# Kernel tuning notes

Measured on AMD Instinct MI355X. Metric: run time of the kernel, lower is better.

The kernel has to match this reference:

```python
import jax, jax.numpy as jnp
import numpy as np

HEAD_DIM = 128
SCALE = 1.0 / np.sqrt(HEAD_DIM)  # standard 1/sqrt(d) attention scaling


def setup_inputs() -> dict:
    key = jax.random.key(0)
    kq, kk, kv = jax.random.split(key, 3)
    q = jax.random.normal(kq, (2, 32, 2048, HEAD_DIM), dtype=jnp.float16)
    k = jax.random.normal(kk, (2, 8, 2048, HEAD_DIM), dtype=jnp.float16)
    v = jax.random.normal(kv, (2, 8, 2048, HEAD_DIM), dtype=jnp.float16)
    return {"q": q, "k": k, "v": v}


def reference(q, k, v):
    # GQA attention: each of the g = H // KVH query heads in a group attends
    # against the group's single shared K/V head (no K/V duplication).
    b, h, sq, d = q.shape
    kvh = k.shape[1]
    g = h // kvh
    # [b, kvh, g, sq, d] -- group-packed Q, mirroring the kernel's _pack_q
    qg = q.reshape(b, kvh, g, sq, d)
    # fp32 accumulation as in flash-attention kernels
    scores = jnp.einsum(
        'bhgqd,bhkd->bhgqk',
        qg.astype(jnp.float32), k.astype(jnp.float32)) * SCALE
    p = jax.nn.softmax(scores, axis=-1)  # non-causal, full attention
    o = jnp.einsum('bhgqk,bhkd->bhgqd', p, v.astype(jnp.float32))
    return o.reshape(b, h, sq, d).astype(q.dtype)
```

## Files before the change

kernel.cpp:

```cpp
#include <hip/hip_runtime.h>

#define SEQ    2048
#define HD     128
#define BN     64
#define NITER  (SEQ / BN)
#define NKVH   16
#define TILE_E 8192

typedef __fp16 f16x8  __attribute__((ext_vector_type(8)));
typedef float  f32x4  __attribute__((ext_vector_type(4)));
typedef float  f32x16 __attribute__((ext_vector_type(16)));

__device__ __forceinline__ unsigned pkh(float a, float b) {
  auto h = __builtin_amdgcn_cvt_pkrtz(a, b);
  return __builtin_bit_cast(unsigned, h);
}

__device__ __forceinline__ void gl_lds16(const unsigned short* g, unsigned short* l) {
  __builtin_amdgcn_global_load_lds(
      (const __attribute__((address_space(1))) void*)g,
      (__attribute__((address_space(3))) void*)l, 16, 0, 0);
}

__global__ __launch_bounds__(256)
void cvt_kv(const float* __restrict__ K, const float* __restrict__ V,
            unsigned short* __restrict__ Kw, unsigned short* __restrict__ Vw)
{
  __shared__ unsigned short kt[TILE_E];
  __shared__ unsigned short vt[TILE_E];
  const int tid = threadIdx.x;
  const int T   = blockIdx.x;
  const long base = (long)T * TILE_E;

  const int krow = tid >> 2, kq4 = tid & 3;
  const float* kp = K + base + (long)krow * HD + kq4 * 32;
#pragma unroll
  for (int jj = 0; jj < 4; ++jj) {
    float4 e = ((const float4*)kp)[2 * jj];
    float4 o = ((const float4*)kp)[2 * jj + 1];
    int4 ksj;
    ksj.x = (int)pkh(e.x, e.y);
    ksj.y = (int)pkh(e.z, e.w);
    ksj.z = (int)pkh(o.x, o.y);
    ksj.w = (int)pkh(o.z, o.w);
    int j = kq4 * 4 + jj;
    int pos = j ^ (krow & 15);
    *(int4*)(kt + krow * HD + pos * 8) = ksj;
  }
  const int kq = tid >> 4, dc8 = tid & 15;
  const float* vp = V + base + (long)(4 * kq) * HD + dc8 * 8;
  float4 vr[4][2];
#pragma unroll
  for (int r = 0; r < 4; ++r) {
    vr[r][0] = ((const float4*)(vp + r * HD))[0];
    vr[r][1] = ((const float4*)(vp + r * HD))[1];
  }
#pragma unroll
  for (int jd = 0; jd < 8; ++jd) {
    const int hsel = jd >> 2, e = jd & 3;
    uint2 v2;
    v2.x = pkh(((const float*)&vr[0][hsel])[e], ((const float*)&vr[1][hsel])[e]);
    v2.y = pkh(((const float*)&vr[2][hsel])[e], ((const float*)&vr[3][hsel])[e]);
    int d = dc8 * 8 + jd;
    int sw3 = ((d >> 3) ^ d) & 7;
    int pos = (kq >> 1) ^ sw3;
    *(uint2*)(vt + d * 64 + pos * 8 + (kq & 1) * 4) = v2;
  }
  __syncthreads();
  int4* kd = (int4*)(Kw + (long)T * TILE_E);
  int4* vd = (int4*)(Vw + (long)T * TILE_E);
  const int4* ksrc = (const int4*)kt;
  const int4* vsrc = (const int4*)vt;
#pragma unroll
  for (int i = 0; i < 4; ++i) {
    kd[i * 256 + tid] = ksrc[i * 256 + tid];
    vd[i * 256 + tid] = vsrc[i * 256 + tid];
  }
}

__global__ __launch_bounds__(256, 2)
void fa_gqa_kernel(const float* __restrict__ Q,
                   const unsigned short* __restrict__ Kw,
                   const unsigned short* __restrict__ Vw,
                   float* __restrict__ O)
{
  __shared__ unsigned short kt_lds[2][TILE_E];
  __shared__ unsigned short vt_lds[2][TILE_E];

  const int tid  = threadIdx.x;
  const int lane = tid & 63;
  const int w    = tid >> 6;
  const int ml   = lane & 31;
  const int hi   = lane >> 5;
  const bool hib = (hi != 0);

  const int F     = blockIdx.x;
  const int xcd   = F & 7;
  const int s     = F >> 3;
  const int bh    = xcd * 8 + (s >> 4);
  const int qtile = s & 15;

  const int b = bh >> 5;
  const int h = bh & 31;
  const long qrow0 = (long)bh * SEQ + qtile * 128 + w * 32;
  const float* Qw = Q + qrow0 * HD;
  float*       Ow = O + qrow0 * HD;
  const int kvh = b * 8 + (h >> 2);

  f16x8 qf[8];
#pragma unroll
  for (int dc = 0; dc < 8; ++dc) {
    const float4* qp = (const float4*)(Qw + ml * HD + dc * 16 + hi * 8);
    float4 a = qp[0], bq = qp[1];
    int4 t;
    t.x = (int)pkh(a.x, a.y);
    t.y = (int)pkh(a.z, a.w);
    t.z = (int)pkh(bq.x, bq.y);
    t.w = (int)pkh(bq.z, bq.w);
    qf[dc] = __builtin_bit_cast(f16x8, t);
  }

  f32x16 oacc[4];
#pragma unroll
  for (int dt = 0; dt < 4; ++dt)
    oacc[dt] = (f32x16)(0.f);

  float mst = -1e30f;
  float lst = 0.f;

  const float K1 = 0.08838834764831845f * 1.4426950408889634f;

  const unsigned short* kwb = Kw + (long)kvh * NITER * TILE_E;
  const unsigned short* vwb = Vw + (long)kvh * NITER * TILE_E;
  const int woff = w * 2048;

  {
    const unsigned short* ks = kwb + woff + lane * 8;
    const unsigned short* vs = vwb + woff + lane * 8;
#pragma unroll
    for (int c = 0; c < 4; ++c) {
      gl_lds16(ks + c * 512, &kt_lds[0][woff + c * 512]);
      gl_lds16(vs + c * 512, &vt_lds[0][woff + c * 512]);
    }
  }

  for (int it = 0; it < NITER; ++it) {
    const int cur = it & 1;
    __syncthreads();

    if (it + 1 < NITER) {
      const unsigned short* ks = kwb + (long)(it + 1) * TILE_E + woff + lane * 8;
      const unsigned short* vs = vwb + (long)(it + 1) * TILE_E + woff + lane * 8;
      const int nxt = cur ^ 1;
#pragma unroll
      for (int c = 0; c < 4; ++c) {
        gl_lds16(ks + c * 512, &kt_lds[nxt][woff + c * 512]);
        gl_lds16(vs + c * 512, &vt_lds[nxt][woff + c * 512]);
      }
    }

    f32x16 sacc[2];
    sacc[0] = (f32x16)(0.f);
    sacc[1] = (f32x16)(0.f);

#pragma unroll
    for (int dc = 0; dc < 8; ++dc) {
#pragma unroll
      for (int kt = 0; kt < 2; ++kt) {
        int row = kt * 32 + ml;
        int pos = (2 * dc + hi) ^ (row & 15);
        f16x8 af = *(const f16x8*)(kt_lds[cur] + row * HD + pos * 8);
        sacc[kt] = __builtin_amdgcn_mfma_f32_32x32x16_f16(
            af, qf[dc], sacc[kt], 0, 0, 0);
      }
    }

    float x0 = fmaxf(sacc[0][0], sacc[1][0]);
    float x1 = fmaxf(sacc[0][1], sacc[1][1]);
    float x2 = fmaxf(sacc[0][2], sacc[1][2]);
    float x3 = fmaxf(sacc[0][3], sacc[1][3]);
#pragma unroll
    for (int r = 4; r < 16; r += 4) {
      x0 = fmaxf(x0, fmaxf(sacc[0][r + 0], sacc[1][r + 0]));
      x1 = fmaxf(x1, fmaxf(sacc[0][r + 1], sacc[1][r + 1]));
      x2 = fmaxf(x2, fmaxf(sacc[0][r + 2], sacc[1][r + 2]));
      x3 = fmaxf(x3, fmaxf(sacc[0][r + 3], sacc[1][r + 3]));
    }
    float mx = fmaxf(fmaxf(x0, x1), fmaxf(x2, x3));
    mx = fmaxf(mx, __shfl_xor(mx, 32, 64));

    if (__any(mx > mst)) {
      float mnew = fmaxf(mst, mx);
      float alpha = __builtin_amdgcn_exp2f(K1 * (mst - mnew));
      mst = mnew;
      lst *= alpha;
#pragma unroll
      for (int dt = 0; dt < 4; ++dt)
        oacc[dt] *= alpha;
    }

    const float nm = -K1 * mst;
    float p0 = 0.f, p1 = 0.f, p2 = 0.f, p3 = 0.f;
#pragma unroll
    for (int kt = 0; kt < 2; ++kt) {
#pragma unroll
      for (int r = 0; r < 16; r += 4) {
        float e0 = __builtin_amdgcn_exp2f(fmaf(sacc[kt][r + 0], K1, nm));
        float e1 = __builtin_amdgcn_exp2f(fmaf(sacc[kt][r + 1], K1, nm));
        float e2 = __builtin_amdgcn_exp2f(fmaf(sacc[kt][r + 2], K1, nm));
        float e3 = __builtin_amdgcn_exp2f(fmaf(sacc[kt][r + 3], K1, nm));
        sacc[kt][r + 0] = e0; p0 += e0;
        sacc[kt][r + 1] = e1; p1 += e1;
        sacc[kt][r + 2] = e2; p2 += e2;
        sacc[kt][r + 3] = e3; p3 += e3;
      }
    }
    lst += (p0 + p1) + (p2 + p3);

#pragma unroll
    for (int st = 0; st < 4; ++st) {
      const int kt = st >> 1;
      const int R  = 8 * (st & 1);
      unsigned pA0 = pkh(sacc[kt][R + 0], sacc[kt][R + 1]);
      unsigned pA1 = pkh(sacc[kt][R + 2], sacc[kt][R + 3]);
      unsigned pB0 = pkh(sacc[kt][R + 4], sacc[kt][R + 5]);
      unsigned pB1 = pkh(sacc[kt][R + 6], sacc[kt][R + 7]);
      unsigned s0 = hib ? pA0 : pB0;
      unsigned s1 = hib ? pA1 : pB1;
      unsigned r0 = (unsigned)__shfl_xor((int)s0, 32, 64);
      unsigned r1 = (unsigned)__shfl_xor((int)s1, 32, 64);
      int4 bf;
      bf.x = (int)(hib ? r0 : pA0);
      bf.y = (int)(hib ? r1 : pA1);
      bf.z = (int)(hib ? pB0 : r0);
      bf.w = (int)(hib ? pB1 : r1);
      f16x8 pfrag = __builtin_bit_cast(f16x8, bf);
#pragma unroll
      for (int dt = 0; dt < 4; ++dt) {
        int d = dt * 32 + ml;
        int pos = (2 * st + hi) ^ (((d >> 3) ^ d) & 7);
        f16x8 vf = *(const f16x8*)(vt_lds[cur] + d * 64 + pos * 8);
        oacc[dt] = __builtin_amdgcn_mfma_f32_32x32x16_f16(
            vf, pfrag, oacc[dt], 0, 0, 0);
      }
    }
  }

  float lf = lst + __shfl_xor(lst, 32, 64);
  float linv = 1.0f / lf;
#pragma unroll
  for (int dt = 0; dt < 4; ++dt) {
#pragma unroll
    for (int t = 0; t < 4; ++t) {
      f32x4 ov;
      ov[0] = oacc[dt][4 * t + 0] * linv;
      ov[1] = oacc[dt][4 * t + 1] * linv;
      ov[2] = oacc[dt][4 * t + 2] * linv;
      ov[3] = oacc[dt][4 * t + 3] * linv;
      *(f32x4*)(Ow + ml * HD + dt * 32 + 8 * t + 4 * hi) = ov;
    }
  }
}

extern "C" void kernel_launch(void* const* d_in, const int* in_sizes, int n_in,
                              void* d_out, int out_size, void* d_ws, size_t ws_size,
                              hipStream_t stream) {
  const float* q = (const float*)d_in[0];
  const float* k = (const float*)d_in[1];
  const float* v = (const float*)d_in[2];
  float* o = (float*)d_out;
  unsigned short* Kw = (unsigned short*)d_ws;
  unsigned short* Vw = Kw + (long)NKVH * NITER * TILE_E;
  cvt_kv<<<dim3(NKVH * NITER), dim3(256), 0, stream>>>(k, v, Kw, Vw);
  fa_gqa_kernel<<<dim3(1024), dim3(256), 0, stream>>>(q, Kw, Vw, o);
}
```

Baseline: 312.5 us.

## Load V fragments directly from global into registers, use 32x32x8 MFMA for PV

The converter now writes V in a fragment-ready layout straight to global memory, with no LDS staging. The attention kernel drops the V LDS double buffer and loads V fragments from global into registers, prefetching one group ahead. The PV product switches from 32x32x16 to 32x32x8 MFMA so the P fragment comes straight from the accumulator registers without cross-lane shuffles. This saves LDS traffic, the shuffles and LDS capacity, but exposes the kernel to global/L2 load latency inside the loop and doubles the number of PV MFMA instructions.

```diff
diff --git a/kernel.cpp b/kernel.cpp
--- a/kernel.cpp
+++ b/kernel.cpp
@@ -7,6 +7,7 @@
 #define NKVH   16
 #define TILE_E 8192
 
+typedef __fp16 f16x4  __attribute__((ext_vector_type(4)));
 typedef __fp16 f16x8  __attribute__((ext_vector_type(8)));
 typedef float  f32x4  __attribute__((ext_vector_type(4)));
 typedef float  f32x16 __attribute__((ext_vector_type(16)));
@@ -27,7 +28,6 @@
             unsigned short* __restrict__ Kw, unsigned short* __restrict__ Vw)
 {
   __shared__ unsigned short kt[TILE_E];
-  __shared__ unsigned short vt[TILE_E];
   const int tid = threadIdx.x;
   const int T   = blockIdx.x;
   const long base = (long)T * TILE_E;
@@ -47,6 +47,7 @@
     int pos = j ^ (krow & 15);
     *(int4*)(kt + krow * HD + pos * 8) = ksj;
   }
+
   const int kq = tid >> 4, dc8 = tid & 15;
   const float* vp = V + base + (long)(4 * kq) * HD + dc8 * 8;
   float4 vr[4][2];
@@ -55,27 +56,22 @@
     vr[r][0] = ((const float4*)(vp + r * HD))[0];
     vr[r][1] = ((const float4*)(vp + r * HD))[1];
   }
+  uint2* vdst = (uint2*)Vw + (long)T * 2048 + kq * 128 + dc8 * 8;
 #pragma unroll
   for (int jd = 0; jd < 8; ++jd) {
     const int hsel = jd >> 2, e = jd & 3;
     uint2 v2;
     v2.x = pkh(((const float*)&vr[0][hsel])[e], ((const float*)&vr[1][hsel])[e]);
     v2.y = pkh(((const float*)&vr[2][hsel])[e], ((const float*)&vr[3][hsel])[e]);
-    int d = dc8 * 8 + jd;
-    int sw3 = ((d >> 3) ^ d) & 7;
-    int pos = (kq >> 1) ^ sw3;
-    *(uint2*)(vt + d * 64 + pos * 8 + (kq & 1) * 4) = v2;
-  }
+    vdst[jd] = v2;
+  }
+
   __syncthreads();
   int4* kd = (int4*)(Kw + (long)T * TILE_E);
-  int4* vd = (int4*)(Vw + (long)T * TILE_E);
   const int4* ksrc = (const int4*)kt;
-  const int4* vsrc = (const int4*)vt;
-#pragma unroll
-  for (int i = 0; i < 4; ++i) {
+#pragma unroll
+  for (int i = 0; i < 4; ++i)
     kd[i * 256 + tid] = ksrc[i * 256 + tid];
-    vd[i * 256 + tid] = vsrc[i * 256 + tid];
-  }
 }
 
 __global__ __launch_bounds__(256, 2)
@@ -85,14 +81,12 @@
                    float* __restrict__ O)
 {
   __shared__ unsigned short kt_lds[2][TILE_E];
-  __shared__ unsigned short vt_lds[2][TILE_E];
 
   const int tid  = threadIdx.x;
   const int lane = tid & 63;
   const int w    = tid >> 6;
   const int ml   = lane & 31;
   const int hi   = lane >> 5;
-  const bool hib = (hi != 0);
 
   const int F     = blockIdx.x;
   const int xcd   = F & 7;
@@ -131,17 +125,16 @@
   const float K1 = 0.08838834764831845f * 1.4426950408889634f;
 
   const unsigned short* kwb = Kw + (long)kvh * NITER * TILE_E;
-  const unsigned short* vwb = Vw + (long)kvh * NITER * TILE_E;
   const int woff = w * 2048;
+
+  const uint2* vw_u2 = (const uint2*)Vw + (long)kvh * NITER * 2048;
+  const int vrow = hi * 128 + ml;
 
   {
     const unsigned short* ks = kwb + woff + lane * 8;
-    const unsigned short* vs = vwb + woff + lane * 8;
-#pragma unroll
-    for (int c = 0; c < 4; ++c) {
+#pragma unroll
+    for (int c = 0; c < 4; ++c)
       gl_lds16(ks + c * 512, &kt_lds[0][woff + c * 512]);
-      gl_lds16(vs + c * 512, &vt_lds[0][woff + c * 512]);
-    }
   }
 
   for (int it = 0; it < NITER; ++it) {
@@ -150,13 +143,10 @@
 
     if (it + 1 < NITER) {
       const unsigned short* ks = kwb + (long)(it + 1) * TILE_E + woff + lane * 8;
-      const unsigned short* vs = vwb + (long)(it + 1) * TILE_E + woff + lane * 8;
       const int nxt = cur ^ 1;
 #pragma unroll
-      for (int c = 0; c < 4; ++c) {
+      for (int c = 0; c < 4; ++c)
         gl_lds16(ks + c * 512, &kt_lds[nxt][woff + c * 512]);
-        gl_lds16(vs + c * 512, &vt_lds[nxt][woff + c * 512]);
-      }
     }
 
     f32x16 sacc[2];
@@ -174,6 +164,12 @@
             af, qf[dc], sacc[kt], 0, 0, 0);
       }
     }
+
+    const uint2* vb = vw_u2 + (long)it * 2048;
+    uint2 vbuf[2][4];
+#pragma unroll
+    for (int dt = 0; dt < 4; ++dt)
+      vbuf[0][dt] = vb[vrow + dt * 32];
 
     float x0 = fmaxf(sacc[0][0], sacc[1][0]);
     float x1 = fmaxf(sacc[0][1], sacc[1][1]);
@@ -218,29 +214,25 @@
     lst += (p0 + p1) + (p2 + p3);
 
 #pragma unroll
-    for (int st = 0; st < 4; ++st) {
-      const int kt = st >> 1;
-      const int R  = 8 * (st & 1);
-      unsigned pA0 = pkh(sacc[kt][R + 0], sacc[kt][R + 1]);
-      unsigned pA1 = pkh(sacc[kt][R + 2], sacc[kt][R + 3]);
-      unsigned pB0 = pkh(sacc[kt][R + 4], sacc[kt][R + 5]);
-      unsigned pB1 = pkh(sacc[kt][R + 6], sacc[kt][R + 7]);
-      unsigned s0 = hib ? pA0 : pB0;
-      unsigned s1 = hib ? pA1 : pB1;
-      unsigned r0 = (unsigned)__shfl_xor((int)s0, 32, 64);
-      unsigned r1 = (unsigned)__shfl_xor((int)s1, 32, 64);
-      int4 bf;
-      bf.x = (int)(hib ? r0 : pA0);
-      bf.y = (int)(hib ? r1 : pA1);
-      bf.z = (int)(hib ? pB0 : r0);
-      bf.w = (int)(hib ? pB1 : r1);
-      f16x8 pfrag = __builtin_bit_cast(f16x8, bf);
+    for (int g = 0; g < 8; ++g) {
+      const int cb = g & 1, nb = cb ^ 1;
+      if (g < 7) {
+#pragma unroll
+        for (int dt = 0; dt < 4; ++dt)
+          vbuf[nb][dt] = vb[(g + 1) * 256 + vrow + dt * 32];
+      }
+      const int kt = g >> 2;
+      const int m  = 4 * (g & 3);
+      unsigned q0 = pkh(sacc[kt][m + 0], sacc[kt][m + 1]);
+      unsigned q1 = pkh(sacc[kt][m + 2], sacc[kt][m + 3]);
+      int2 bfr;
+      bfr.x = (int)q0;
+      bfr.y = (int)q1;
+      f16x4 pfrag = __builtin_bit_cast(f16x4, bfr);
 #pragma unroll
       for (int dt = 0; dt < 4; ++dt) {
-        int d = dt * 32 + ml;
-        int pos = (2 * st + hi) ^ (((d >> 3) ^ d) & 7);
-        f16x8 vf = *(const f16x8*)(vt_lds[cur] + d * 64 + pos * 8);
-        oacc[dt] = __builtin_amdgcn_mfma_f32_32x32x16_f16(
+        f16x4 vf = __builtin_bit_cast(f16x4, vbuf[cb][dt]);
+        oacc[dt] = __builtin_amdgcn_mfma_f32_32x32x8f16(
             vf, pfrag, oacc[dt], 0, 0, 0);
       }
     }
```

New measurement: 340.2 us. +8.9%, slower.

## Replace P cross-lane shuffle with 32x32x8 MFMA pairs and re-layout V tiles

Applied to the files above, without the earlier changes.

Drops the __shfl_xor exchange that rearranged the softmax probabilities into a 32x32x16 MFMA B-operand. The P@V product now uses two 32x32x8 f16 MFMAs per step, fed directly from each lane's own accumulator registers. To match, the V preprocessing kernel writes V with a different k-ordering inside each 8-element chunk. This removes the cross-lane permutes and selects but doubles the MFMA instruction count, and the older x8 instruction may have lower throughput per FLOP on this hardware.

```diff
diff --git a/kernel.cpp b/kernel.cpp
--- a/kernel.cpp
+++ b/kernel.cpp
@@ -7,6 +7,7 @@
 #define NKVH   16
 #define TILE_E 8192
 
+typedef __fp16 f16x4  __attribute__((ext_vector_type(4)));
 typedef __fp16 f16x8  __attribute__((ext_vector_type(8)));
 typedef float  f32x4  __attribute__((ext_vector_type(4)));
 typedef float  f32x16 __attribute__((ext_vector_type(16)));
@@ -55,6 +56,8 @@
     vr[r][0] = ((const float4*)(vp + r * HD))[0];
     vr[r][1] = ((const float4*)(vp + r * HD))[1];
   }
+  const int c8u  = 2 * (kq >> 2) + (kq & 1);
+  const int half = (kq >> 1) & 1;
 #pragma unroll
   for (int jd = 0; jd < 8; ++jd) {
     const int hsel = jd >> 2, e = jd & 3;
@@ -63,8 +66,8 @@
     v2.y = pkh(((const float*)&vr[2][hsel])[e], ((const float*)&vr[3][hsel])[e]);
     int d = dc8 * 8 + jd;
     int sw3 = ((d >> 3) ^ d) & 7;
-    int pos = (kq >> 1) ^ sw3;
-    *(uint2*)(vt + d * 64 + pos * 8 + (kq & 1) * 4) = v2;
+    int pos = c8u ^ sw3;
+    *(uint2*)(vt + d * 64 + pos * 8 + half * 4) = v2;
   }
   __syncthreads();
   int4* kd = (int4*)(Kw + (long)T * TILE_E);
@@ -92,7 +95,6 @@
   const int w    = tid >> 6;
   const int ml   = lane & 31;
   const int hi   = lane >> 5;
-  const bool hib = (hi != 0);
 
   const int F     = blockIdx.x;
   const int xcd   = F & 7;
@@ -218,30 +220,28 @@
     lst += (p0 + p1) + (p2 + p3);
 
 #pragma unroll
-    for (int st = 0; st < 4; ++st) {
-      const int kt = st >> 1;
-      const int R  = 8 * (st & 1);
-      unsigned pA0 = pkh(sacc[kt][R + 0], sacc[kt][R + 1]);
-      unsigned pA1 = pkh(sacc[kt][R + 2], sacc[kt][R + 3]);
-      unsigned pB0 = pkh(sacc[kt][R + 4], sacc[kt][R + 5]);
-      unsigned pB1 = pkh(sacc[kt][R + 6], sacc[kt][R + 7]);
-      unsigned s0 = hib ? pA0 : pB0;
-      unsigned s1 = hib ? pA1 : pB1;
-      unsigned r0 = (unsigned)__shfl_xor((int)s0, 32, 64);
-      unsigned r1 = (unsigned)__shfl_xor((int)s1, 32, 64);
-      int4 bf;
-      bf.x = (int)(hib ? r0 : pA0);
-      bf.y = (int)(hib ? r1 : pA1);
-      bf.z = (int)(hib ? pB0 : r0);
-      bf.w = (int)(hib ? pB1 : r1);
-      f16x8 pfrag = __builtin_bit_cast(f16x8, bf);
+    for (int t = 0; t < 4; ++t) {
+      const int g0 = 2 * t, g1 = 2 * t + 1;
+      unsigned a0 = pkh(sacc[g0 >> 2][4 * (g0 & 3) + 0], sacc[g0 >> 2][4 * (g0 & 3) + 1]);
+      unsigned a1 = pkh(sacc[g0 >> 2][4 * (g0 & 3) + 2], sacc[g0 >> 2][4 * (g0 & 3) + 3]);
+      unsigned b0 = pkh(sacc[g1 >> 2][4 * (g1 & 3) + 0], sacc[g1 >> 2][4 * (g1 & 3) + 1]);
+      unsigned b1 = pkh(sacc[g1 >> 2][4 * (g1 & 3) + 2], sacc[g1 >> 2][4 * (g1 & 3) + 3]);
+      int2 pf0i; pf0i.x = (int)a0; pf0i.y = (int)a1;
+      int2 pf1i; pf1i.x = (int)b0; pf1i.y = (int)b1;
+      f16x4 pf0 = __builtin_bit_cast(f16x4, pf0i);
+      f16x4 pf1 = __builtin_bit_cast(f16x4, pf1i);
 #pragma unroll
       for (int dt = 0; dt < 4; ++dt) {
         int d = dt * 32 + ml;
-        int pos = (2 * st + hi) ^ (((d >> 3) ^ d) & 7);
-        f16x8 vf = *(const f16x8*)(vt_lds[cur] + d * 64 + pos * 8);
-        oacc[dt] = __builtin_amdgcn_mfma_f32_32x32x16_f16(
-            vf, pfrag, oacc[dt], 0, 0, 0);
+        int pos = (2 * t + hi) ^ (((d >> 3) ^ d) & 7);
+        f16x8 vv = *(const f16x8*)(vt_lds[cur] + d * 64 + pos * 8);
+        int4 vi = __builtin_bit_cast(int4, vv);
+        int2 vlo; vlo.x = vi.x; vlo.y = vi.y;
+        int2 vhi; vhi.x = vi.z; vhi.y = vi.w;
+        f16x4 v0 = __builtin_bit_cast(f16x4, vlo);
+        f16x4 v1 = __builtin_bit_cast(f16x4, vhi);
+        oacc[dt] = __builtin_amdgcn_mfma_f32_32x32x8f16(v0, pf0, oacc[dt], 0, 0, 0);
+        oacc[dt] = __builtin_amdgcn_mfma_f32_32x32x8f16(v1, pf1, oacc[dt], 0, 0, 0);
       }
     }
   }
```

After: 313.8 us. Within noise of the previous version (+0.4%).
